# Kernel optimization log

Measured on AMD Instinct MI355X. Metric: run time of the kernel, lower is better.

Reference implementation:

```python
import jax, jax.numpy as jnp
import numpy as np

B, L, S, H = 8, 128, 160, 768      # batch, words, wordpieces, bert hidden
T, CD = 16, 50                      # max chars per word, char embed/lstm dim
WV, WD = 50000, 100                 # word vocab, word embed dim
CV = 128                            # char vocab
NEG = -1e30


def _run_lstm(x, w_ih, w_hh, b):
    # x: [N, T, D] -> hidden states [N, T, Hc]; torch LSTM gate order i,f,g,o
    N = x.shape[0]
    Hc = w_hh.shape[1]
    def step(carry, xt):
        h, c = carry
        g = xt @ w_ih.T + h @ w_hh.T + b
        i, f, gg, o = jnp.split(g, 4, axis=-1)
        c = jax.nn.sigmoid(f) * c + jax.nn.sigmoid(i) * jnp.tanh(gg)
        h = jax.nn.sigmoid(o) * jnp.tanh(c)
        return (h, c), h
    init = (jnp.zeros((N, Hc), x.dtype), jnp.zeros((N, Hc), x.dtype))
    _, hs = jax.lax.scan(step, init, jnp.swapaxes(x, 0, 1))
    return jnp.swapaxes(hs, 0, 1)


def setup_inputs() -> dict:
    key = jax.random.key(0)
    ks = jax.random.split(key, 14)
    sc = 1.0 / np.sqrt(CD)
    return {
        "bert_emb": jax.random.normal(ks[0], (B, S, H), jnp.float32),
        "pieces2word": jax.random.randint(ks[1], (B, L, S), 0, 2, jnp.int32),
        "word_ids": jax.random.randint(ks[2], (B, L), 0, WV),
        "char_ids": jax.random.randint(ks[3], (B, L, T), 0, CV),
        "char_count": jax.random.randint(ks[4], (B, L), 0, T, jnp.int32),
        "token_masks_char": jax.random.randint(ks[5], (B, L, T), 0, 2, jnp.int32),
        "word_table": jax.random.normal(ks[6], (WV, WD), jnp.float32) * 0.02,
        "char_table": jax.random.normal(ks[7], (CV, CD), jnp.float32) * 0.02,
        "w_ih_f": jax.random.uniform(ks[8], (4 * CD, CD), jnp.float32, -sc, sc),
        "w_hh_f": jax.random.uniform(ks[9], (4 * CD, CD), jnp.float32, -sc, sc),
        "b_f": jax.random.uniform(ks[10], (4 * CD,), jnp.float32, -sc, sc),
        "w_ih_b": jax.random.uniform(ks[11], (4 * CD, CD), jnp.float32, -sc, sc),
        "w_hh_b": jax.random.uniform(ks[12], (4 * CD, CD), jnp.float32, -sc, sc),
        "b_b": jax.random.uniform(ks[13], (4 * CD,), jnp.float32, -sc, sc),
    }


def reference(bert_emb, pieces2word, word_ids, char_ids, char_count,
              token_masks_char, word_table, char_table,
              w_ih_f, w_hh_f, b_f, w_ih_b, w_hh_b, b_b):
    cls_embedding = bert_emb[:, 0]                      # [B, H]
    # piece -> word max pooling (masked fill with global min, then max)
    min_value = jax.lax.stop_gradient(jnp.min(bert_emb))
    expanded = jnp.where(pieces2word[:, :, :, None] != 0,
                         bert_emb[:, None, :, :], min_value)  # [B, L, S, H]
    word_reps = jnp.max(expanded, axis=2)               # [B, L, H]

    # word embedding lookup (emb_dropout is identity in eval)
    word_embed = word_table[word_ids]                   # [B, L, WD]

    # char biLSTM
    N = B * L
    lengths = jnp.maximum(char_count.reshape(N), 1)     # char_count[==0] = 1
    x = char_table[char_ids.reshape(N, T)]              # [N, T, CD]
    h_fwd = _run_lstm(x, w_ih_f, w_hh_f, b_f)           # [N, T, CD]
    # reverse each sequence by its true length (packed-sequence semantics)
    t = jnp.arange(T)
    rev_idx = lengths[:, None] - 1 - t[None, :]         # [N, T]
    valid = (rev_idx >= 0).astype(x.dtype)[:, :, None]
    gidx = jnp.clip(rev_idx, 0, T - 1)[:, :, None]
    x_rev = jnp.take_along_axis(x, gidx, axis=1) * valid
    h_rev = _run_lstm(x_rev, w_ih_b, w_hh_b, b_b)
    h_bwd = jnp.take_along_axis(h_rev, gidx, axis=1) * valid  # un-reverse + zero pad
    char_h = jnp.concatenate([h_fwd, h_bwd], axis=-1).reshape(B, L, T, 2 * CD)

    # combine(..., 'max'): additive -1e30 mask, max over chars, zero all-masked
    m = jnp.where(token_masks_char[:, :, :, None] == 0, NEG, 0.0).astype(char_h.dtype)
    h_token_char = jnp.max(m + char_h, axis=2)
    h_token_char = jnp.where(h_token_char == NEG, 0.0, h_token_char)  # [B, L, 2CD]

    embeds = jnp.concatenate([word_reps, word_embed, h_token_char], axis=-1)
    return embeds, cls_embedding
```

## Files before the change

kernel.cpp:

```cpp
#include <hip/hip_runtime.h>

#define B_   8
#define L_   128
#define S_   160
#define H_   768
#define T_   16
#define CD_  50
#define WD_  100
#define NGATE 200
#define NEGV (-1e30f)
#define FMAXV 3.402823466e+38f
#define NELEM (B_ * S_ * H_)

typedef short  s16x8 __attribute__((ext_vector_type(8)));
typedef float  f32x4 __attribute__((ext_vector_type(4)));

__device__ __forceinline__ unsigned short f2bf(float f) {
    unsigned u = __float_as_uint(f);
    u = (u + 0x7FFFu + ((u >> 16) & 1u)) >> 16;
    return (unsigned short)u;
}
__device__ __forceinline__ float sigm(float x) {
    return __fdividef(1.f, 1.f + __expf(-x));
}
__device__ __forceinline__ float tanh_fast(float x) {
    float a = fabsf(x);
    float e = __expf(-2.f * a);
    float t = __fdividef(1.f - e, 1.f + e);
    return copysignf(t, x);
}
__device__ __forceinline__ float4 fmax4(float4 a, float4 b) {
    return make_float4(fmaxf(a.x, b.x), fmaxf(a.y, b.y), fmaxf(a.z, b.z), fmaxf(a.w, b.w));
}

struct LstmS {
    s16x8 xall[T_][128];
    s16x8 hbuf[2][128];
    int   slen[16], smask[16];
};
struct WordS {
    int list[S_ + 8];
    int cnt;
    float red[256];
};
#define SMEM_BYTES 37120

__device__ void lstm_body(int unit, char* smem,
        const int* __restrict__ char_ids, const int* __restrict__ char_count,
        const int* __restrict__ tok_mask, const float* __restrict__ char_table,
        const float* __restrict__ w_ih_f, const float* __restrict__ w_hh_f,
        const float* __restrict__ b_f,
        const float* __restrict__ w_ih_b, const float* __restrict__ w_hh_b,
        const float* __restrict__ b_b,
        float* __restrict__ out) {
    LstmS& sh = *(LstmS*)smem;
    const int dir  = unit >> 6;
    const int grp  = unit & 63;
    const int tid  = threadIdx.x;
    const int lane = tid & 63;
    const int wv   = tid >> 6;

    if (tid < 16) {
        int n = grp * 16 + tid;
        int c = char_count[n];
        sh.slen[tid] = (c > 0) ? c : 1;
        int mb = 0;
        for (int t = 0; t < T_; ++t) mb |= (tok_mask[n * T_ + t] != 0) << t;
        sh.smask[tid] = mb;
    }
    { s16x8 z = {0,0,0,0,0,0,0,0};
      if (tid < 128) sh.hbuf[0][tid] = z; else sh.hbuf[1][tid - 128] = z; }

    const int m   = lane & 3;
    const int k2  = (lane >> 2) & 3;
    const int q   = lane >> 4;
    const int sstar = q * 4 + m;

    const float* WI = dir ? w_ih_b : w_ih_f;
    const float* WH = dir ? w_hh_b : w_hh_f;
    const float* BV = dir ? b_b    : b_f;
    const int cnt = (wv == 0) ? 4 : 3;
    int   ccol[4];
    int   cvld[4];
    int   hofs[4];
    float bv[4];
    s16x8 bf[4][4];
#pragma unroll
    for (int i = 0; i < 4; ++i) {
        int nt = (i < 3) ? (wv + 4 * i) : 12;
        int c  = nt * 4 + k2;
        int jv = (i < cnt) && (c < 50);
        ccol[i] = c;
        cvld[i] = jv;
        hofs[i] = ((c >> 3) * 16 + sstar) * 8 + (c & 7);
        int orow = m * 50 + c;
        bv[i] = jv ? BV[orow] : 0.f;
        const float* wi = WI + orow * CD_;
        const float* wh = WH + orow * CD_;
#pragma unroll
        for (int kt = 0; kt < 4; ++kt) {
            int kst = kt * 32 + q * 8;
            s16x8 fr = {0,0,0,0,0,0,0,0};
#pragma unroll
            for (int e = 0; e < 8; ++e) {
                int k = kst + e;
                float v = 0.f;
                if (jv) {
                    if (k < 64) { if (k < CD_) v = wi[k]; }
                    else        { int kk = k - 64; if (kk < CD_) v = wh[kk]; }
                }
                fr[e] = (short)f2bf(v);
            }
            bf[i][kt] = fr;
        }
    }
    __syncthreads();

    for (int idx = tid; idx < T_ * 128; idx += 256) {
        int t = idx >> 7;
        int u = idx & 127;
        int g = u >> 4, s = u & 15;
        int st = dir ? (sh.slen[s] - 1 - t) : t;
        s16x8 fr = {0,0,0,0,0,0,0,0};
        if (st >= 0) {
            int cidv = char_ids[(grp * 16 + s) * T_ + st];
            const float* row = char_table + cidv * CD_;
            int kbase = g * 8;
#pragma unroll
            for (int e = 0; e < 8; ++e) {
                int k = kbase + e;
                if (k < CD_) fr[e] = (short)f2bf(row[k]);
            }
        }
        sh.xall[t][u] = fr;
    }

    const int laneofs = (q << 4) + (lane & 15);
    const int sl_s = sh.slen[sstar];
    const int sm_s = sh.smask[sstar];

    float cst0 = 0.f, cst1 = 0.f, cst2 = 0.f, cst3 = 0.f;
    float mr0 = NEGV, mr1 = NEGV, mr2 = NEGV, mr3 = NEGV;
    const bool m0 = (lane & 1) != 0;
    const bool m1 = (lane & 2) != 0;

    __syncthreads();

#define TRUPD(I, D) { \
    float v0 = (D)[0], v1 = (D)[1], v2 = (D)[2], v3 = (D)[3]; \
    float s10 = __shfl_xor(v0, 1), s11 = __shfl_xor(v1, 1); \
    float s12 = __shfl_xor(v2, 1), s13 = __shfl_xor(v3, 1); \
    float A0 = m0 ? s11 : v0; \
    float A1 = m0 ? v1 : s10; \
    float A2 = m0 ? s13 : v2; \
    float A3 = m0 ? v3 : s12; \
    float s20 = __shfl_xor(A0, 2), s21 = __shfl_xor(A1, 2); \
    float s22 = __shfl_xor(A2, 2), s23 = __shfl_xor(A3, 2); \
    float gi = m1 ? s22 : A0; \
    float gf = m1 ? s23 : A1; \
    float gg = m1 ? A2 : s20; \
    float go = m1 ? A3 : s21; \
    float cc = sigm(gf) * cst##I + sigm(gi) * tanh_fast(gg); \
    float h  = sigm(go) * tanh_fast(cc); \
    if (cvld[I]) { \
        cst##I = cc; \
        hw[hofs[I]] = f2bf(h); \
        int tt = dir ? (sl_s - 1 - t) : t; \
        if (tt >= 0 && ((sm_s >> tt) & 1)) mr##I = fmaxf(mr##I, h); \
    } }

#pragma unroll 1
    for (int t = 0; t < T_; ++t) {
        const int cur = t & 1, nxt = cur ^ 1;
        unsigned short* hw = (unsigned short*)&sh.hbuf[nxt][0];
        const s16x8* xb = sh.xall[t];
        s16x8 a0 = xb[laneofs];
        s16x8 a1 = xb[64 + laneofs];
        s16x8 a2 = sh.hbuf[cur][laneofs];
        s16x8 a3 = sh.hbuf[cur][64 + laneofs];

        {
            f32x4 d0 = {bv[0], bv[0], bv[0], bv[0]};
            f32x4 d1 = {bv[1], bv[1], bv[1], bv[1]};
            d0 = __builtin_amdgcn_mfma_f32_16x16x32_bf16(a0, bf[0][0], d0, 0, 0, 0);
            d1 = __builtin_amdgcn_mfma_f32_16x16x32_bf16(a0, bf[1][0], d1, 0, 0, 0);
            d0 = __builtin_amdgcn_mfma_f32_16x16x32_bf16(a1, bf[0][1], d0, 0, 0, 0);
            d1 = __builtin_amdgcn_mfma_f32_16x16x32_bf16(a1, bf[1][1], d1, 0, 0, 0);
            d0 = __builtin_amdgcn_mfma_f32_16x16x32_bf16(a2, bf[0][2], d0, 0, 0, 0);
            d1 = __builtin_amdgcn_mfma_f32_16x16x32_bf16(a2, bf[1][2], d1, 0, 0, 0);
            d0 = __builtin_amdgcn_mfma_f32_16x16x32_bf16(a3, bf[0][3], d0, 0, 0, 0);
            d1 = __builtin_amdgcn_mfma_f32_16x16x32_bf16(a3, bf[1][3], d1, 0, 0, 0);
            TRUPD(0, d0)
            TRUPD(1, d1)
        }
        {
            f32x4 d2 = {bv[2], bv[2], bv[2], bv[2]};
            d2 = __builtin_amdgcn_mfma_f32_16x16x32_bf16(a0, bf[2][0], d2, 0, 0, 0);
            d2 = __builtin_amdgcn_mfma_f32_16x16x32_bf16(a1, bf[2][1], d2, 0, 0, 0);
            d2 = __builtin_amdgcn_mfma_f32_16x16x32_bf16(a2, bf[2][2], d2, 0, 0, 0);
            d2 = __builtin_amdgcn_mfma_f32_16x16x32_bf16(a3, bf[2][3], d2, 0, 0, 0);
            TRUPD(2, d2)
            if (cnt == 4) {
                f32x4 d3 = {bv[3], bv[3], bv[3], bv[3]};
                d3 = __builtin_amdgcn_mfma_f32_16x16x32_bf16(a0, bf[3][0], d3, 0, 0, 0);
                d3 = __builtin_amdgcn_mfma_f32_16x16x32_bf16(a1, bf[3][1], d3, 0, 0, 0);
                d3 = __builtin_amdgcn_mfma_f32_16x16x32_bf16(a2, bf[3][2], d3, 0, 0, 0);
                d3 = __builtin_amdgcn_mfma_f32_16x16x32_bf16(a3, bf[3][3], d3, 0, 0, 0);
                TRUPD(3, d3)
            }
        }
        __syncthreads();
    }

    float* ob = out + (size_t)(grp * 16 + sstar) * 968 + 868 + dir * CD_;
#define OUTW(I) if (cvld[I]) { \
    float mm = mr##I; \
    if (dir && (sm_s >> sl_s)) mm = fmaxf(mm, 0.f); \
    if (mm == NEGV) mm = 0.f; \
    ob[ccol[I]] = mm; }
    OUTW(0) OUTW(1) OUTW(2) OUTW(3)
}

__device__ void word_body(int bl, char* smem,
        const float* __restrict__ bert, const int* __restrict__ p2w,
        const int* __restrict__ word_ids, const float* __restrict__ word_table,
        float* __restrict__ out) {
    WordS& sh = *(WordS*)smem;
    int b = bl >> 7;
    int l = bl & 127;
    int tid = threadIdx.x;

    if (tid == 0) sh.cnt = 0;
    __syncthreads();
    if (tid < S_) {
        if (p2w[bl * S_ + tid]) {
            int p = atomicAdd(&sh.cnt, 1);
            sh.list[p] = tid;
        }
    }
    __syncthreads();
    int n = sh.cnt;

    float* orow = out + (size_t)bl * 968;

    if (n > 0) {
        if (tid < ((8 - (n & 7)) & 7)) sh.list[n + tid] = sh.list[0];
        __syncthreads();
        int n8 = (n + 7) & ~7;
        if (tid < 192) {
            const float4* bb = (const float4*)(bert + (size_t)b * S_ * H_) + tid;
            float4 mx = make_float4(-FMAXV, -FMAXV, -FMAXV, -FMAXV);
            for (int i = 0; i < n8; i += 8) {
                float4 v0 = bb[(size_t)sh.list[i]     * 192];
                float4 v1 = bb[(size_t)sh.list[i + 1] * 192];
                float4 v2 = bb[(size_t)sh.list[i + 2] * 192];
                float4 v3 = bb[(size_t)sh.list[i + 3] * 192];
                float4 v4 = bb[(size_t)sh.list[i + 4] * 192];
                float4 v5 = bb[(size_t)sh.list[i + 5] * 192];
                float4 v6 = bb[(size_t)sh.list[i + 6] * 192];
                float4 v7 = bb[(size_t)sh.list[i + 7] * 192];
                mx = fmax4(mx, fmax4(fmax4(fmax4(v0, v1), fmax4(v2, v3)),
                                     fmax4(fmax4(v4, v5), fmax4(v6, v7))));
            }
            ((float4*)orow)[tid] = mx;
        } else {
            int j = tid - 192;
            int wid = word_ids[bl];
            orow[768 + j] = word_table[(size_t)wid * WD_ + j];
            if (j < WD_ - 64) orow[768 + 64 + j] = word_table[(size_t)wid * WD_ + 64 + j];
        }
    } else {
        float mv = FMAXV;
        const float4* x4 = (const float4*)bert;
        for (int i = tid; i < NELEM / 4; i += 256) {
            float4 v = x4[i];
            mv = fminf(mv, fminf(fminf(v.x, v.y), fminf(v.z, v.w)));
        }
        sh.red[tid] = mv;
        __syncthreads();
        for (int o = 128; o > 0; o >>= 1) {
            if (tid < o) sh.red[tid] = fminf(sh.red[tid], sh.red[tid + o]);
            __syncthreads();
        }
        float g = sh.red[0];
        if (tid < 192) {
            ((float4*)orow)[tid] = make_float4(g, g, g, g);
        } else {
            int j = tid - 192;
            int wid = word_ids[bl];
            orow[768 + j] = word_table[(size_t)wid * WD_ + j];
            if (j < WD_ - 64) orow[768 + 64 + j] = word_table[(size_t)wid * WD_ + 64 + j];
        }
    }

    if (l == 0 && tid < 192) {
        const float4* c4 = (const float4*)(bert + (size_t)b * S_ * H_);
        float4* co = (float4*)(out + (size_t)B_ * L_ * 968 + (size_t)b * H_);
        co[tid] = c4[tid];
    }
}

__global__ __launch_bounds__(256, 3) void kmega(
        const float* __restrict__ bert, const int* __restrict__ p2w,
        const int* __restrict__ word_ids, const int* __restrict__ char_ids,
        const int* __restrict__ char_count, const int* __restrict__ tok_mask,
        const float* __restrict__ word_table, const float* __restrict__ char_table,
        const float* __restrict__ w_ih_f, const float* __restrict__ w_hh_f,
        const float* __restrict__ b_f,
        const float* __restrict__ w_ih_b, const float* __restrict__ w_hh_b,
        const float* __restrict__ b_b,
        float* __restrict__ out) {
    __shared__ __align__(16) char smem[SMEM_BYTES];
    int bid = blockIdx.x;
    if (bid < 128) {
        lstm_body(bid, smem, char_ids, char_count, tok_mask, char_table,
                  w_ih_f, w_hh_f, b_f, w_ih_b, w_hh_b, b_b, out);
    } else {
        word_body(bid - 128, smem, bert, p2w, word_ids, word_table, out);
    }
}

extern "C" void kernel_launch(void* const* d_in, const int* in_sizes, int n_in,
                              void* d_out, int out_size, void* d_ws, size_t ws_size,
                              hipStream_t stream) {
    const float* bert       = (const float*)d_in[0];
    const int*   p2w        = (const int*)d_in[1];
    const int*   word_ids   = (const int*)d_in[2];
    const int*   char_ids   = (const int*)d_in[3];
    const int*   char_count = (const int*)d_in[4];
    const int*   tok_mask   = (const int*)d_in[5];
    const float* word_table = (const float*)d_in[6];
    const float* char_table = (const float*)d_in[7];
    const float* w_ih_f = (const float*)d_in[8];
    const float* w_hh_f = (const float*)d_in[9];
    const float* b_f    = (const float*)d_in[10];
    const float* w_ih_b = (const float*)d_in[11];
    const float* w_hh_b = (const float*)d_in[12];
    const float* b_b    = (const float*)d_in[13];

    float* out = (float*)d_out;

    kmega<<<128 + B_ * L_, 256, 0, stream>>>(bert, p2w, word_ids, char_ids, char_count, tok_mask,
                                             word_table, char_table,
                                             w_ih_f, w_hh_f, b_f, w_ih_b, w_hh_b, b_b, out);
}
```

Before: 44.95 us.

## Split mega-kernel into LSTM and word kernels, stage weights in swizzled LDS

Splits the fused kernel into two launches: an LSTM kernel and a word-pooling kernel. The LSTM kernel now converts the gate weights to bf16 once into XOR-swizzled shared memory and reads MFMA B fragments from LDS each step, where before it kept them as 64 register values per thread. This is meant to cut register pressure and speed up weight loading. In exchange it adds LDS reads to every recurrent step and a second launch, and the two kernels now run back-to-back on one stream instead of overlapping.

New measurement: 64.79 us. 44.2% more time.

```diff
diff --git a/kernel.cpp b/kernel.cpp
--- a/kernel.cpp
+++ b/kernel.cpp
@@ -15,6 +15,15 @@
 typedef short  s16x8 __attribute__((ext_vector_type(8)));
 typedef float  f32x4 __attribute__((ext_vector_type(4)));
 
+#define WBF_OFF    0
+#define WBF_BYTES  (NGATE * 256)
+#define XALL_OFF   (WBF_OFF + WBF_BYTES)
+#define XALL_BYTES (T_ * 128 * 16)
+#define HBUF_OFF   (XALL_OFF + XALL_BYTES)
+#define HBUF_BYTES (2 * 128 * 16)
+#define META_OFF   (HBUF_OFF + HBUF_BYTES)
+#define SMEM_TOTAL (META_OFF + 32 * 4)
+
 __device__ __forceinline__ unsigned short f2bf(float f) {
     unsigned u = __float_as_uint(f);
     u = (u + 0x7FFFu + ((u >> 16) & 1u)) >> 16;
@@ -33,19 +42,7 @@
     return make_float4(fmaxf(a.x, b.x), fmaxf(a.y, b.y), fmaxf(a.z, b.z), fmaxf(a.w, b.w));
 }
 
-struct LstmS {
-    s16x8 xall[T_][128];
-    s16x8 hbuf[2][128];
-    int   slen[16], smask[16];
-};
-struct WordS {
-    int list[S_ + 8];
-    int cnt;
-    float red[256];
-};
-#define SMEM_BYTES 37120
-
-__device__ void lstm_body(int unit, char* smem,
+__global__ __launch_bounds__(256, 1) void klstm_mfma(
         const int* __restrict__ char_ids, const int* __restrict__ char_count,
         const int* __restrict__ tok_mask, const float* __restrict__ char_table,
         const float* __restrict__ w_ih_f, const float* __restrict__ w_hh_f,
@@ -53,74 +50,49 @@
         const float* __restrict__ w_ih_b, const float* __restrict__ w_hh_b,
         const float* __restrict__ b_b,
         float* __restrict__ out) {
-    LstmS& sh = *(LstmS*)smem;
+    extern __shared__ __align__(16) char smem[];
+    unsigned short* wb16 = (unsigned short*)(smem + WBF_OFF);
+    s16x8*          xal  = (s16x8*)(smem + XALL_OFF);
+    s16x8*          hb   = (s16x8*)(smem + HBUF_OFF);
+    int*            slen = (int*)(smem + META_OFF);
+    int*            smask = slen + 16;
+
+    const int unit = blockIdx.x;
     const int dir  = unit >> 6;
     const int grp  = unit & 63;
     const int tid  = threadIdx.x;
     const int lane = tid & 63;
     const int wv   = tid >> 6;
 
+    const float* WI = dir ? w_ih_b : w_ih_f;
+    const float* WH = dir ? w_hh_b : w_hh_f;
+    const float* BV = dir ? b_b    : b_f;
+
     if (tid < 16) {
         int n = grp * 16 + tid;
         int c = char_count[n];
-        sh.slen[tid] = (c > 0) ? c : 1;
+        slen[tid] = (c > 0) ? c : 1;
         int mb = 0;
         for (int t = 0; t < T_; ++t) mb |= (tok_mask[n * T_ + t] != 0) << t;
-        sh.smask[tid] = mb;
+        smask[tid] = mb;
     }
     { s16x8 z = {0,0,0,0,0,0,0,0};
-      if (tid < 128) sh.hbuf[0][tid] = z; else sh.hbuf[1][tid - 128] = z; }
-
-    const int m   = lane & 3;
-    const int k2  = (lane >> 2) & 3;
-    const int q   = lane >> 4;
-    const int sstar = q * 4 + m;
-
-    const float* WI = dir ? w_ih_b : w_ih_f;
-    const float* WH = dir ? w_hh_b : w_hh_f;
-    const float* BV = dir ? b_b    : b_f;
-    const int cnt = (wv == 0) ? 4 : 3;
-    int   ccol[4];
-    int   cvld[4];
-    int   hofs[4];
-    float bv[4];
-    s16x8 bf[4][4];
-#pragma unroll
-    for (int i = 0; i < 4; ++i) {
-        int nt = (i < 3) ? (wv + 4 * i) : 12;
-        int c  = nt * 4 + k2;
-        int jv = (i < cnt) && (c < 50);
-        ccol[i] = c;
-        cvld[i] = jv;
-        hofs[i] = ((c >> 3) * 16 + sstar) * 8 + (c & 7);
-        int orow = m * 50 + c;
-        bv[i] = jv ? BV[orow] : 0.f;
-        const float* wi = WI + orow * CD_;
-        const float* wh = WH + orow * CD_;
-#pragma unroll
-        for (int kt = 0; kt < 4; ++kt) {
-            int kst = kt * 32 + q * 8;
-            s16x8 fr = {0,0,0,0,0,0,0,0};
-#pragma unroll
-            for (int e = 0; e < 8; ++e) {
-                int k = kst + e;
-                float v = 0.f;
-                if (jv) {
-                    if (k < 64) { if (k < CD_) v = wi[k]; }
-                    else        { int kk = k - 64; if (kk < CD_) v = wh[kk]; }
-                }
-                fr[e] = (short)f2bf(v);
-            }
-            bf[i][kt] = fr;
-        }
-    }
+      if (tid < 256) { hb[tid] = z; }
+      for (int i = tid; i < WBF_BYTES / 16; i += 256) ((s16x8*)wb16)[i] = z; }
     __syncthreads();
+
+    for (int idx = tid; idx < NGATE * CD_; idx += 256) {
+        int j = idx / CD_, k = idx - j * CD_;
+        int sw = (j & 7) << 4;
+        wb16[(j * 256 + ((k * 2) ^ sw)) >> 1]        = f2bf(WI[idx]);
+        wb16[(j * 256 + (((64 + k) * 2) ^ sw)) >> 1] = f2bf(WH[idx]);
+    }
 
     for (int idx = tid; idx < T_ * 128; idx += 256) {
         int t = idx >> 7;
         int u = idx & 127;
         int g = u >> 4, s = u & 15;
-        int st = dir ? (sh.slen[s] - 1 - t) : t;
+        int st = dir ? (slen[s] - 1 - t) : t;
         s16x8 fr = {0,0,0,0,0,0,0,0};
         if (st >= 0) {
             int cidv = char_ids[(grp * 16 + s) * T_ + st];
@@ -132,12 +104,39 @@
                 if (k < CD_) fr[e] = (short)f2bf(row[k]);
             }
         }
-        sh.xall[t][u] = fr;
+        xal[t * 128 + u] = fr;
+    }
+
+    const int m   = lane & 3;
+    const int k2  = (lane >> 2) & 3;
+    const int q   = lane >> 4;
+    const int sstar = q * 4 + m;
+    const int cnt = (wv == 0) ? 4 : 3;
+
+    int   ccol[4], cvld[4], hofs[4], ba[4][4];
+    float bv[4];
+#pragma unroll
+    for (int i = 0; i < 4; ++i) {
+        int nt = (i < 3) ? (wv + 4 * i) : 12;
+        int c  = nt * 4 + k2;
+        int jv = (i < cnt) && (c < CD_);
+        ccol[i] = c;
+        cvld[i] = jv;
+        hofs[i] = ((c >> 3) * 16 + sstar) * 8 + (c & 7);
+        int orow = m * 50 + c;
+        bv[i] = jv ? BV[orow] : 0.f;
+        int ora = (orow > NGATE - 1) ? (NGATE - 1) : orow;
+        int sw  = (ora & 7) << 4;
+#pragma unroll
+        for (int kt = 0; kt < 4; ++kt) {
+            int col = kt * 32 + q * 8;
+            ba[i][kt] = ora * 256 + ((col * 2) ^ sw);
+        }
     }
 
     const int laneofs = (q << 4) + (lane & 15);
-    const int sl_s = sh.slen[sstar];
-    const int sm_s = sh.smask[sstar];
+    const int sl_s = slen[sstar];
+    const int sm_s = smask[sstar];
 
     float cst0 = 0.f, cst1 = 0.f, cst2 = 0.f, cst3 = 0.f;
     float mr0 = NEGV, mr1 = NEGV, mr2 = NEGV, mr3 = NEGV;
@@ -145,6 +144,9 @@
     const bool m1 = (lane & 2) != 0;
 
     __syncthreads();
+
+    const char* wb = (const char*)wb16;
+#define BFR(I, KT) (*(const s16x8*)(wb + ba[I][KT]))
 
 #define TRUPD(I, D) { \
     float v0 = (D)[0], v1 = (D)[1], v2 = (D)[2], v3 = (D)[3]; \
@@ -172,40 +174,40 @@
 #pragma unroll 1
     for (int t = 0; t < T_; ++t) {
         const int cur = t & 1, nxt = cur ^ 1;
-        unsigned short* hw = (unsigned short*)&sh.hbuf[nxt][0];
-        const s16x8* xb = sh.xall[t];
+        unsigned short* hw = (unsigned short*)(smem + HBUF_OFF) + nxt * 1024;
+        const s16x8* xb = xal + t * 128;
         s16x8 a0 = xb[laneofs];
         s16x8 a1 = xb[64 + laneofs];
-        s16x8 a2 = sh.hbuf[cur][laneofs];
-        s16x8 a3 = sh.hbuf[cur][64 + laneofs];
+        s16x8 a2 = hb[cur * 128 + laneofs];
+        s16x8 a3 = hb[cur * 128 + 64 + laneofs];
 
         {
             f32x4 d0 = {bv[0], bv[0], bv[0], bv[0]};
             f32x4 d1 = {bv[1], bv[1], bv[1], bv[1]};
-            d0 = __builtin_amdgcn_mfma_f32_16x16x32_bf16(a0, bf[0][0], d0, 0, 0, 0);
-            d1 = __builtin_amdgcn_mfma_f32_16x16x32_bf16(a0, bf[1][0], d1, 0, 0, 0);
-            d0 = __builtin_amdgcn_mfma_f32_16x16x32_bf16(a1, bf[0][1], d0, 0, 0, 0);
-            d1 = __builtin_amdgcn_mfma_f32_16x16x32_bf16(a1, bf[1][1], d1, 0, 0, 0);
-            d0 = __builtin_amdgcn_mfma_f32_16x16x32_bf16(a2, bf[0][2], d0, 0, 0, 0);
-            d1 = __builtin_amdgcn_mfma_f32_16x16x32_bf16(a2, bf[1][2], d1, 0, 0, 0);
-            d0 = __builtin_amdgcn_mfma_f32_16x16x32_bf16(a3, bf[0][3], d0, 0, 0, 0);
-            d1 = __builtin_amdgcn_mfma_f32_16x16x32_bf16(a3, bf[1][3], d1, 0, 0, 0);
+            d0 = __builtin_amdgcn_mfma_f32_16x16x32_bf16(a0, BFR(0,0), d0, 0, 0, 0);
+            d1 = __builtin_amdgcn_mfma_f32_16x16x32_bf16(a0, BFR(1,0), d1, 0, 0, 0);
+            d0 = __builtin_amdgcn_mfma_f32_16x16x32_bf16(a1, BFR(0,1), d0, 0, 0, 0);
+            d1 = __builtin_amdgcn_mfma_f32_16x16x32_bf16(a1, BFR(1,1), d1, 0, 0, 0);
+            d0 = __builtin_amdgcn_mfma_f32_16x16x32_bf16(a2, BFR(0,2), d0, 0, 0, 0);
+            d1 = __builtin_amdgcn_mfma_f32_16x16x32_bf16(a2, BFR(1,2), d1, 0, 0, 0);
+            d0 = __builtin_amdgcn_mfma_f32_16x16x32_bf16(a3, BFR(0,3), d0, 0, 0, 0);
+            d1 = __builtin_amdgcn_mfma_f32_16x16x32_bf16(a3, BFR(1,3), d1, 0, 0, 0);
             TRUPD(0, d0)
             TRUPD(1, d1)
         }
         {
             f32x4 d2 = {bv[2], bv[2], bv[2], bv[2]};
-            d2 = __builtin_amdgcn_mfma_f32_16x16x32_bf16(a0, bf[2][0], d2, 0, 0, 0);
-            d2 = __builtin_amdgcn_mfma_f32_16x16x32_bf16(a1, bf[2][1], d2, 0, 0, 0);
-            d2 = __builtin_amdgcn_mfma_f32_16x16x32_bf16(a2, bf[2][2], d2, 0, 0, 0);
-            d2 = __builtin_amdgcn_mfma_f32_16x16x32_bf16(a3, bf[2][3], d2, 0, 0, 0);
+            d2 = __builtin_amdgcn_mfma_f32_16x16x32_bf16(a0, BFR(2,0), d2, 0, 0, 0);
+            d2 = __builtin_amdgcn_mfma_f32_16x16x32_bf16(a1, BFR(2,1), d2, 0, 0, 0);
+            d2 = __builtin_amdgcn_mfma_f32_16x16x32_bf16(a2, BFR(2,2), d2, 0, 0, 0);
+            d2 = __builtin_amdgcn_mfma_f32_16x16x32_bf16(a3, BFR(2,3), d2, 0, 0, 0);
             TRUPD(2, d2)
             if (cnt == 4) {
                 f32x4 d3 = {bv[3], bv[3], bv[3], bv[3]};
-                d3 = __builtin_amdgcn_mfma_f32_16x16x32_bf16(a0, bf[3][0], d3, 0, 0, 0);
-                d3 = __builtin_amdgcn_mfma_f32_16x16x32_bf16(a1, bf[3][1], d3, 0, 0, 0);
-                d3 = __builtin_amdgcn_mfma_f32_16x16x32_bf16(a2, bf[3][2], d3, 0, 0, 0);
-                d3 = __builtin_amdgcn_mfma_f32_16x16x32_bf16(a3, bf[3][3], d3, 0, 0, 0);
+                d3 = __builtin_amdgcn_mfma_f32_16x16x32_bf16(a0, BFR(3,0), d3, 0, 0, 0);
+                d3 = __builtin_amdgcn_mfma_f32_16x16x32_bf16(a1, BFR(3,1), d3, 0, 0, 0);
+                d3 = __builtin_amdgcn_mfma_f32_16x16x32_bf16(a2, BFR(3,2), d3, 0, 0, 0);
+                d3 = __builtin_amdgcn_mfma_f32_16x16x32_bf16(a3, BFR(3,3), d3, 0, 0, 0);
                 TRUPD(3, d3)
             }
         }
@@ -221,44 +223,46 @@
     OUTW(0) OUTW(1) OUTW(2) OUTW(3)
 }
 
-__device__ void word_body(int bl, char* smem,
-        const float* __restrict__ bert, const int* __restrict__ p2w,
-        const int* __restrict__ word_ids, const float* __restrict__ word_table,
-        float* __restrict__ out) {
-    WordS& sh = *(WordS*)smem;
+__global__ __launch_bounds__(256) void kword(const float* __restrict__ bert, const int* __restrict__ p2w,
+                                             const int* __restrict__ word_ids, const float* __restrict__ word_table,
+                                             float* __restrict__ out) {
+    __shared__ int list[S_ + 8];
+    __shared__ int cnt;
+    __shared__ float red[256];
+    int bl = blockIdx.x;
     int b = bl >> 7;
     int l = bl & 127;
     int tid = threadIdx.x;
 
-    if (tid == 0) sh.cnt = 0;
+    if (tid == 0) cnt = 0;
     __syncthreads();
     if (tid < S_) {
         if (p2w[bl * S_ + tid]) {
-            int p = atomicAdd(&sh.cnt, 1);
-            sh.list[p] = tid;
+            int p = atomicAdd(&cnt, 1);
+            list[p] = tid;
         }
     }
     __syncthreads();
-    int n = sh.cnt;
+    int n = cnt;
 
     float* orow = out + (size_t)bl * 968;
 
     if (n > 0) {
-        if (tid < ((8 - (n & 7)) & 7)) sh.list[n + tid] = sh.list[0];
+        if (tid < ((8 - (n & 7)) & 7)) list[n + tid] = list[0];
         __syncthreads();
         int n8 = (n + 7) & ~7;
         if (tid < 192) {
             const float4* bb = (const float4*)(bert + (size_t)b * S_ * H_) + tid;
             float4 mx = make_float4(-FMAXV, -FMAXV, -FMAXV, -FMAXV);
             for (int i = 0; i < n8; i += 8) {
-                float4 v0 = bb[(size_t)sh.list[i]     * 192];
-                float4 v1 = bb[(size_t)sh.list[i + 1] * 192];
-                float4 v2 = bb[(size_t)sh.list[i + 2] * 192];
-                float4 v3 = bb[(size_t)sh.list[i + 3] * 192];
-                float4 v4 = bb[(size_t)sh.list[i + 4] * 192];
-                float4 v5 = bb[(size_t)sh.list[i + 5] * 192];
-                float4 v6 = bb[(size_t)sh.list[i + 6] * 192];
-                float4 v7 = bb[(size_t)sh.list[i + 7] * 192];
+                float4 v0 = bb[(size_t)list[i]     * 192];
+                float4 v1 = bb[(size_t)list[i + 1] * 192];
+                float4 v2 = bb[(size_t)list[i + 2] * 192];
+                float4 v3 = bb[(size_t)list[i + 3] * 192];
+                float4 v4 = bb[(size_t)list[i + 4] * 192];
+                float4 v5 = bb[(size_t)list[i + 5] * 192];
+                float4 v6 = bb[(size_t)list[i + 6] * 192];
+                float4 v7 = bb[(size_t)list[i + 7] * 192];
                 mx = fmax4(mx, fmax4(fmax4(fmax4(v0, v1), fmax4(v2, v3)),
                                      fmax4(fmax4(v4, v5), fmax4(v6, v7))));
             }
@@ -276,13 +280,13 @@
             float4 v = x4[i];
             mv = fminf(mv, fminf(fminf(v.x, v.y), fminf(v.z, v.w)));
         }
-        sh.red[tid] = mv;
+        red[tid] = mv;
         __syncthreads();
         for (int o = 128; o > 0; o >>= 1) {
-            if (tid < o) sh.red[tid] = fminf(sh.red[tid], sh.red[tid + o]);
+            if (tid < o) red[tid] = fminf(red[tid], red[tid + o]);
             __syncthreads();
         }
-        float g = sh.red[0];
+        float g = red[0];
         if (tid < 192) {
             ((float4*)orow)[tid] = make_float4(g, g, g, g);
         } else {
@@ -297,26 +301,6 @@
         const float4* c4 = (const float4*)(bert + (size_t)b * S_ * H_);
         float4* co = (float4*)(out + (size_t)B_ * L_ * 968 + (size_t)b * H_);
         co[tid] = c4[tid];
-    }
-}
-
-__global__ __launch_bounds__(256, 3) void kmega(
-        const float* __restrict__ bert, const int* __restrict__ p2w,
-        const int* __restrict__ word_ids, const int* __restrict__ char_ids,
-        const int* __restrict__ char_count, const int* __restrict__ tok_mask,
-        const float* __restrict__ word_table, const float* __restrict__ char_table,
-        const float* __restrict__ w_ih_f, const float* __restrict__ w_hh_f,
-        const float* __restrict__ b_f,
-        const float* __restrict__ w_ih_b, const float* __restrict__ w_hh_b,
-        const float* __restrict__ b_b,
-        float* __restrict__ out) {
-    __shared__ __align__(16) char smem[SMEM_BYTES];
-    int bid = blockIdx.x;
-    if (bid < 128) {
-        lstm_body(bid, smem, char_ids, char_count, tok_mask, char_table,
-                  w_ih_f, w_hh_f, b_f, w_ih_b, w_hh_b, b_b, out);
-    } else {
-        word_body(bid - 128, smem, bert, p2w, word_ids, word_table, out);
     }
 }
 
@@ -340,7 +324,7 @@
 
     float* out = (float*)d_out;
 
-    kmega<<<128 + B_ * L_, 256, 0, stream>>>(bert, p2w, word_ids, char_ids, char_count, tok_mask,
-                                             word_table, char_table,
-                                             w_ih_f, w_hh_f, b_f, w_ih_b, w_hh_b, b_b, out);
-}
+    klstm_mfma<<<128, 256, SMEM_TOTAL, stream>>>(char_ids, char_count, tok_mask, char_table,
+                                                 w_ih_f, w_hh_f, b_f, w_ih_b, w_hh_b, b_b, out);
+    kword<<<B_ * L_, 256, 0, stream>>>(bert, p2w, word_ids, word_table, out);
+}
```
